# Kernel optimization log

Measured on AMD Instinct MI355X. Metric: run time of the kernel, lower is better.

## Reference

```python
import jax, jax.numpy as jnp
import numpy as np

N = 100000
E = 1600000
F = 64
THETA = (0.6, -0.4, 0.3, -0.2, 0.1)  # k = 5 polynomial coefficients


def setup_inputs() -> dict:
    key = jax.random.key(0)
    kx, ke = jax.random.split(key)
    x = jax.random.normal(kx, (N, F), dtype=jnp.float32)
    edge_index = jax.random.randint(ke, (2, E), 0, N, dtype=jnp.int64)
    return {"x": x, "edge_index": edge_index}


def _l_sym_mul(feat, src, dst, deg_inv_sqrt, n):
    # L_sym * feat = feat - D^{-1/2} A D^{-1/2} feat
    src_norm = feat[src] * deg_inv_sqrt[src]            # [E, F] gather + scale
    agg = jax.ops.segment_sum(src_norm, dst, num_segments=n)  # scatter-add to dst
    return feat - deg_inv_sqrt * agg


def reference(x, edge_index):
    src, dst = edge_index[0], edge_index[1]
    n = x.shape[0]
    # in-degree from dst, clamp to >= 1, D^{-1/2} as [N, 1]
    deg = jax.ops.segment_sum(jnp.ones((src.shape[0],), dtype=x.dtype), dst,
                              num_segments=n)
    deg = jnp.maximum(deg, 1.0)[:, None]
    deg_inv_sqrt = deg ** -0.5

    h_acc = THETA[0] * x
    feat = x
    for k in range(1, len(THETA)):
        feat = _l_sym_mul(feat, src, dst, deg_inv_sqrt, n)
        h_acc = h_acc + THETA[k] * feat
    return h_acc
```

## Files before the change

kernel.cpp:

```cpp
#include <hip/hip_runtime.h>


constexpr int kF = 64;
constexpr int BSHIFT = 8;
constexpr int NB = 1 << BSHIFT;
constexpr int TILE = 2048;
constexpr int KMAX = 512;

static __device__ __forceinline__ float bfl(unsigned u) {
    return __uint_as_float(u << 16);
}
static __device__ __forceinline__ float bfh(unsigned u) {
    return __uint_as_float(u & 0xffff0000u);
}
static __device__ __forceinline__ unsigned f2bf(float f) {
    unsigned u = __float_as_uint(f);
    return (u + 0x7fffu + ((u >> 16) & 1u)) >> 16;
}
static __device__ __forceinline__ unsigned pack2(float a, float b) {
    return f2bf(a) | (f2bf(b) << 16);
}

__global__ void k_binA(const int* __restrict__ src, const int* __restrict__ dst,
                       unsigned* __restrict__ pairs, int* __restrict__ gcursor,
                       const float4* __restrict__ x4, uint4* __restrict__ xb4,
                       int n8, int E, int K, int cap) {
    __shared__ int hist[KMAX];
    __shared__ int gb[KMAX];
    const int tid = threadIdx.x;
    const long long tb = (long long)blockIdx.x * TILE;
    const int tcount = (int)min((long long)TILE, (long long)E - tb);

    {
        int per = (n8 + gridDim.x - 1) / (int)gridDim.x;
        int b0 = blockIdx.x * per;
        int b1 = min(b0 + per, n8);
        for (int i = b0 + tid; i < b1; i += 512) {
            float4 a = x4[2 * i];
            float4 b = x4[2 * i + 1];
            uint4 o;
            o.x = pack2(a.x, a.y);
            o.y = pack2(a.z, a.w);
            o.z = pack2(b.x, b.y);
            o.w = pack2(b.z, b.w);
            xb4[i] = o;
        }
    }

    hist[tid] = 0;
    __syncthreads();
    int dc[4], sc[4];
    #pragma unroll
    for (int k = 0; k < 4; ++k) {
        int i = tid + k * 512;
        if (i < tcount) {
            dc[k] = dst[tb + i];
            sc[k] = src[tb + i];
            atomicAdd(&hist[dc[k] >> BSHIFT], 1);
        } else {
            dc[k] = -1;
        }
    }
    __syncthreads();
    int hv = hist[tid];
    gb[tid] = (tid < K && hv > 0) ? atomicAdd(&gcursor[tid], hv) : 0;
    hist[tid] = 0;
    __syncthreads();
    #pragma unroll
    for (int k = 0; k < 4; ++k) {
        if (dc[k] >= 0) {
            int d = dc[k];
            int b = d >> BSHIFT;
            int pos = atomicAdd(&hist[b], 1);
            pairs[(size_t)b * cap + gb[b] + pos] =
                ((unsigned)(d & (NB - 1)) << 23) | (unsigned)sc[k];
        }
    }
}

__global__ void k_binB1(const unsigned* __restrict__ pairs, const int* __restrict__ gcursor,
                        int* __restrict__ rp, float* __restrict__ dinv,
                        int N, int E, int K, int cap) {
    __shared__ int gsc[KMAX];
    __shared__ int cnt[NB];
    __shared__ int stmp[NB];
    const int b = blockIdx.x;
    const int tid = threadIdx.x;

    int gv = (tid < K) ? gcursor[tid] : 0;
    gsc[tid] = gv;
    __syncthreads();
    for (int o = 1; o < KMAX; o <<= 1) {
        int t = (tid >= o) ? gsc[tid - o] : 0;
        __syncthreads();
        gsc[tid] += t;
        __syncthreads();
    }
    const int ecnt = gcursor[b];
    const int base = gsc[b] - ecnt;
    const unsigned* bp = pairs + (size_t)b * cap;

    if (tid < NB) cnt[tid] = 0;
    __syncthreads();
    for (int i = tid; i < ecnt; i += 512)
        atomicAdd(&cnt[bp[i] >> 23], 1);
    __syncthreads();
    int v = (tid < NB) ? cnt[tid] : 0;
    if (tid < NB) stmp[tid] = v;
    __syncthreads();
    for (int o = 1; o < NB; o <<= 1) {
        int t = (tid >= o && tid < NB) ? stmp[tid - o] : 0;
        __syncthreads();
        if (tid < NB) stmp[tid] += t;
        __syncthreads();
    }
    int node = (b << BSHIFT) + tid;
    if (tid < NB && node < N) {
        rp[node] = base + stmp[tid] - v;
        dinv[node] = rsqrtf(fmaxf((float)v, 1.0f));
    }
    if (b == K - 1 && tid == 0) rp[N] = E;
}

__global__ void k_binB2(const unsigned* __restrict__ pairs, const int* __restrict__ gcursor,
                        const int* __restrict__ rp, const float* __restrict__ dinv,
                        int2* __restrict__ ecsr, int N, int K, int cap) {
    __shared__ int cur[NB];
    const int b = blockIdx.x;
    const int tid = threadIdx.x;
    const int ecnt = gcursor[b];
    const unsigned* bp = pairs + (size_t)b * cap;

    int node = (b << BSHIFT) + tid;
    if (tid < NB) cur[tid] = (node < N) ? rp[node] : 0;
    __syncthreads();
    for (int i = tid; i < ecnt; i += 512) {
        unsigned p = bp[i];
        int s = (int)(p & 0x7FFFFFu);
        int pos = atomicAdd(&cur[p >> 23], 1);
        ecsr[pos] = make_int2(s, __float_as_int(dinv[s]));
    }
}

__global__ void k_gather(const int* __restrict__ rp, const int2* __restrict__ ecsr,
                         const unsigned short* __restrict__ featin,
                         const float* __restrict__ dinv,
                         unsigned short* __restrict__ featout, int n) {
    int wid = (blockIdx.x * blockDim.x + threadIdx.x) >> 6;
    int lane = threadIdx.x & 63;
    int half = lane >> 5;
    int r = (lane >> 3) & 3;
    int c = lane & 7;
    int node = wid * 2 + half;
    if (wid * 2 >= n) return;
    bool valid = node < n;
    int beg = valid ? rp[node] : 0;
    int end = valid ? rp[node + 1] : 0;
    int len = end - beg;
    int olen = __shfl_xor(len, 32, 64);
    int mlen = (len > olen) ? len : olen;

    float acc[8] = {0.f, 0.f, 0.f, 0.f, 0.f, 0.f, 0.f, 0.f};
    for (int i = 0; i < mlen; i += 16) {
        int j1 = beg + i + r;
        int j2 = j1 + 4;
        int j3 = j1 + 8;
        int j4 = j1 + 12;
        bool ok1 = j1 < end, ok2 = j2 < end, ok3 = j3 < end, ok4 = j4 < end;
        int2 e1 = ecsr[ok1 ? j1 : 0];
        int2 e2 = ecsr[ok2 ? j2 : 0];
        int2 e3 = ecsr[ok3 ? j3 : 0];
        int2 e4 = ecsr[ok4 ? j4 : 0];
        float w1 = ok1 ? __int_as_float(e1.y) : 0.0f;
        float w2 = ok2 ? __int_as_float(e2.y) : 0.0f;
        float w3 = ok3 ? __int_as_float(e3.y) : 0.0f;
        float w4 = ok4 ? __int_as_float(e4.y) : 0.0f;
        uint4 ra = *(const uint4*)(featin + ((size_t)e1.x << 6) + (c << 3));
        uint4 rb = *(const uint4*)(featin + ((size_t)e2.x << 6) + (c << 3));
        uint4 rc = *(const uint4*)(featin + ((size_t)e3.x << 6) + (c << 3));
        uint4 rd = *(const uint4*)(featin + ((size_t)e4.x << 6) + (c << 3));
        acc[0] += w1 * bfl(ra.x); acc[1] += w1 * bfh(ra.x);
        acc[2] += w1 * bfl(ra.y); acc[3] += w1 * bfh(ra.y);
        acc[4] += w1 * bfl(ra.z); acc[5] += w1 * bfh(ra.z);
        acc[6] += w1 * bfl(ra.w); acc[7] += w1 * bfh(ra.w);
        acc[0] += w2 * bfl(rb.x); acc[1] += w2 * bfh(rb.x);
        acc[2] += w2 * bfl(rb.y); acc[3] += w2 * bfh(rb.y);
        acc[4] += w2 * bfl(rb.z); acc[5] += w2 * bfh(rb.z);
        acc[6] += w2 * bfl(rb.w); acc[7] += w2 * bfh(rb.w);
        acc[0] += w3 * bfl(rc.x); acc[1] += w3 * bfh(rc.x);
        acc[2] += w3 * bfl(rc.y); acc[3] += w3 * bfh(rc.y);
        acc[4] += w3 * bfl(rc.z); acc[5] += w3 * bfh(rc.z);
        acc[6] += w3 * bfl(rc.w); acc[7] += w3 * bfh(rc.w);
        acc[0] += w4 * bfl(rd.x); acc[1] += w4 * bfh(rd.x);
        acc[2] += w4 * bfl(rd.y); acc[3] += w4 * bfh(rd.y);
        acc[4] += w4 * bfl(rd.z); acc[5] += w4 * bfh(rd.z);
        acc[6] += w4 * bfl(rd.w); acc[7] += w4 * bfh(rd.w);
    }
    #pragma unroll
    for (int m = 8; m <= 16; m <<= 1) {
        #pragma unroll
        for (int i = 0; i < 8; ++i)
            acc[i] += __shfl_xor(acc[i], m, 64);
    }

    if (r == 0 && valid) {
        size_t off = ((size_t)node << 6) + (c << 3);
        uint4 rr = *(const uint4*)(featin + off);
        float di = dinv[node];
        uint4 o;
        o.x = pack2(bfl(rr.x) - di * acc[0], bfh(rr.x) - di * acc[1]);
        o.y = pack2(bfl(rr.y) - di * acc[2], bfh(rr.y) - di * acc[3]);
        o.z = pack2(bfl(rr.z) - di * acc[4], bfh(rr.z) - di * acc[5]);
        o.w = pack2(bfl(rr.w) - di * acc[6], bfh(rr.w) - di * acc[7]);
        *(uint4*)(featout + off) = o;
    }
}

__global__ void k_final(const uint4* __restrict__ xb,
                        const uint4* __restrict__ f1, const uint4* __restrict__ f2,
                        const uint4* __restrict__ f3, const uint4* __restrict__ f4,
                        float4* __restrict__ h4, int n8,
                        float t0, float t1, float t2, float t3, float t4) {
    int i = blockIdx.x * blockDim.x + threadIdx.x;
    if (i >= n8) return;
    uint4 xv = xb[i];
    uint4 a = f1[i], b = f2[i], cc = f3[i], d = f4[i];
    float4 h0, h1;
    h0.x = t0 * bfl(xv.x) + t1 * bfl(a.x) + t2 * bfl(b.x) + t3 * bfl(cc.x) + t4 * bfl(d.x);
    h0.y = t0 * bfh(xv.x) + t1 * bfh(a.x) + t2 * bfh(b.x) + t3 * bfh(cc.x) + t4 * bfh(d.x);
    h0.z = t0 * bfl(xv.y) + t1 * bfl(a.y) + t2 * bfl(b.y) + t3 * bfl(cc.y) + t4 * bfl(d.y);
    h0.w = t0 * bfh(xv.y) + t1 * bfh(a.y) + t2 * bfh(b.y) + t3 * bfh(cc.y) + t4 * bfh(d.y);
    h1.x = t0 * bfl(xv.z) + t1 * bfl(a.z) + t2 * bfl(b.z) + t3 * bfl(cc.z) + t4 * bfl(d.z);
    h1.y = t0 * bfh(xv.z) + t1 * bfh(a.z) + t2 * bfh(b.z) + t3 * bfh(cc.z) + t4 * bfh(d.z);
    h1.z = t0 * bfl(xv.w) + t1 * bfl(a.w) + t2 * bfl(b.w) + t3 * bfl(cc.w) + t4 * bfl(d.w);
    h1.w = t0 * bfh(xv.w) + t1 * bfh(a.w) + t2 * bfh(b.w) + t3 * bfh(cc.w) + t4 * bfh(d.w);
    h4[2 * i] = h0;
    h4[2 * i + 1] = h1;
}

extern "C" void kernel_launch(void* const* d_in, const int* in_sizes, int n_in,
                              void* d_out, int out_size, void* d_ws, size_t ws_size,
                              hipStream_t stream) {
    const float* x  = (const float*)d_in[0];
    const int*   ei = (const int*)d_in[1];
    const int N = in_sizes[0] / kF;
    const int E = in_sizes[1] / 2;
    const int* src = ei;
    const int* dst = ei + E;
    float* h = (float*)d_out;

    const int K = (N + NB - 1) >> BSHIFT;
    const int cap = 2 * ((E + K - 1) / K);

    char* ws = (char*)d_ws;
    size_t off = 0;
    auto carve = [&](size_t bytes) {
        void* p = ws + off;
        off = (off + bytes + 511) & ~(size_t)511;
        return p;
    };
    int*            gcursor = (int*)carve((size_t)K * 4);
    int*            rp      = (int*)carve((size_t)(N + 1) * 4);
    float*          dinv    = (float*)carve((size_t)N * 4);
    int2*           ecsr    = (int2*)carve((size_t)E * 8);
    unsigned short* xb      = (unsigned short*)carve((size_t)N * kF * 2);
    unsigned short* f1      = (unsigned short*)carve((size_t)N * kF * 2);
    unsigned short* f2      = (unsigned short*)carve((size_t)N * kF * 2);
    unsigned short* f3      = (unsigned short*)carve((size_t)N * kF * 2);
    unsigned short* f4      = (unsigned short*)carve((size_t)N * kF * 2);
    unsigned*       pairs   = (unsigned*)carve((size_t)K * cap * 4);

    const float theta[5] = {0.6f, -0.4f, 0.3f, -0.2f, 0.1f};
    const int n8 = N * kF / 8;

    hipMemsetAsync(gcursor, 0, (size_t)K * 4, stream);
    k_binA<<<(E + TILE - 1) / TILE, 512, 0, stream>>>(src, dst, pairs, gcursor,
                                                      (const float4*)x, (uint4*)xb,
                                                      n8, E, K, cap);
    k_binB1<<<K, 512, 0, stream>>>(pairs, gcursor, rp, dinv, N, E, K, cap);
    k_binB2<<<K, 512, 0, stream>>>(pairs, gcursor, rp, dinv, ecsr, N, K, cap);

    const int nwaves = (N + 1) / 2;
    const int gblocks = (nwaves + 3) / 4;
    k_gather<<<gblocks, 256, 0, stream>>>(rp, ecsr, xb, dinv, f1, N);
    k_gather<<<gblocks, 256, 0, stream>>>(rp, ecsr, f1, dinv, f2, N);
    k_gather<<<gblocks, 256, 0, stream>>>(rp, ecsr, f2, dinv, f3, N);
    k_gather<<<gblocks, 256, 0, stream>>>(rp, ecsr, f3, dinv, f4, N);

    k_final<<<(n8 + 255) / 256, 256, 0, stream>>>((const uint4*)xb,
                                                  (const uint4*)f1, (const uint4*)f2,
                                                  (const uint4*)f3, (const uint4*)f4,
                                                  (float4*)h, n8,
                                                  theta[0], theta[1], theta[2],
                                                  theta[3], theta[4]);
}
```

Before: 268.0 us.

## Sort nodes by degree for balanced gather and halve per-iteration unroll

Adds a counting sort of nodes by in-degree (histogram, scan, permutation kernels) and has each gather wave process nodes in descending-degree order. Half-waves paired together then have similar edge counts, which reduces idle lanes from the max-length loop. The inner loop now handles 8 edges per iteration instead of 16, so less work is wasted on masked slots. In exchange it launches three extra small kernels, and output writes and self-feature reads become scattered through the permutation.

```diff
diff --git a/kernel.cpp b/kernel.cpp
--- a/kernel.cpp
+++ b/kernel.cpp
@@ -142,7 +142,64 @@
     }
 }
 
-__global__ void k_gather(const int* __restrict__ rp, const int2* __restrict__ ecsr,
+__global__ void k_dhist(const int* __restrict__ rp, int* __restrict__ dhist, int N) {
+    __shared__ int lh[64];
+    int tid = threadIdx.x;
+    int node = blockIdx.x * 256 + tid;
+    if (tid < 64) lh[tid] = 0;
+    __syncthreads();
+    if (node < N) {
+        int d = rp[node + 1] - rp[node];
+        atomicAdd(&lh[63 - min(d, 63)], 1);
+    }
+    __syncthreads();
+    if (tid < 64 && lh[tid] > 0) atomicAdd(&dhist[tid], lh[tid]);
+}
+
+__global__ void k_dscan(const int* __restrict__ dhist, int* __restrict__ dcur) {
+    __shared__ int t[64];
+    int tid = threadIdx.x;
+    int v = dhist[tid];
+    t[tid] = v;
+    __syncthreads();
+    for (int o = 1; o < 64; o <<= 1) {
+        int u = (tid >= o) ? t[tid - o] : 0;
+        __syncthreads();
+        t[tid] += u;
+        __syncthreads();
+    }
+    dcur[tid] = t[tid] - v;
+}
+
+__global__ void k_dperm(const int* __restrict__ rp, int* __restrict__ dcur,
+                        int* __restrict__ perm, int N) {
+    __shared__ int lh[64];
+    __shared__ int lbase[64];
+    __shared__ int lcur[64];
+    int tid = threadIdx.x;
+    int node = blockIdx.x * 256 + tid;
+    if (tid < 64) lh[tid] = 0;
+    __syncthreads();
+    int bin = -1;
+    if (node < N) {
+        int d = rp[node + 1] - rp[node];
+        bin = 63 - min(d, 63);
+        atomicAdd(&lh[bin], 1);
+    }
+    __syncthreads();
+    if (tid < 64) {
+        lbase[tid] = atomicAdd(&dcur[tid], lh[tid]);
+        lcur[tid] = 0;
+    }
+    __syncthreads();
+    if (bin >= 0) {
+        int pos = lbase[bin] + atomicAdd(&lcur[bin], 1);
+        perm[pos] = node;
+    }
+}
+
+__global__ void k_gather(const int* __restrict__ perm, const int* __restrict__ rp,
+                         const int2* __restrict__ ecsr,
                          const unsigned short* __restrict__ featin,
                          const float* __restrict__ dinv,
                          unsigned short* __restrict__ featout, int n) {
@@ -151,9 +208,10 @@
     int half = lane >> 5;
     int r = (lane >> 3) & 3;
     int c = lane & 7;
-    int node = wid * 2 + half;
+    int idx = wid * 2 + half;
     if (wid * 2 >= n) return;
-    bool valid = node < n;
+    bool valid = idx < n;
+    int node = valid ? perm[idx] : 0;
     int beg = valid ? rp[node] : 0;
     int end = valid ? rp[node + 1] : 0;
     int len = end - beg;
@@ -161,24 +219,17 @@
     int mlen = (len > olen) ? len : olen;
 
     float acc[8] = {0.f, 0.f, 0.f, 0.f, 0.f, 0.f, 0.f, 0.f};
-    for (int i = 0; i < mlen; i += 16) {
+    for (int i = 0; i < mlen; i += 8) {
         int j1 = beg + i + r;
         int j2 = j1 + 4;
-        int j3 = j1 + 8;
-        int j4 = j1 + 12;
-        bool ok1 = j1 < end, ok2 = j2 < end, ok3 = j3 < end, ok4 = j4 < end;
+        bool ok1 = j1 < end;
+        bool ok2 = j2 < end;
         int2 e1 = ecsr[ok1 ? j1 : 0];
         int2 e2 = ecsr[ok2 ? j2 : 0];
-        int2 e3 = ecsr[ok3 ? j3 : 0];
-        int2 e4 = ecsr[ok4 ? j4 : 0];
         float w1 = ok1 ? __int_as_float(e1.y) : 0.0f;
         float w2 = ok2 ? __int_as_float(e2.y) : 0.0f;
-        float w3 = ok3 ? __int_as_float(e3.y) : 0.0f;
-        float w4 = ok4 ? __int_as_float(e4.y) : 0.0f;
         uint4 ra = *(const uint4*)(featin + ((size_t)e1.x << 6) + (c << 3));
         uint4 rb = *(const uint4*)(featin + ((size_t)e2.x << 6) + (c << 3));
-        uint4 rc = *(const uint4*)(featin + ((size_t)e3.x << 6) + (c << 3));
-        uint4 rd = *(const uint4*)(featin + ((size_t)e4.x << 6) + (c << 3));
         acc[0] += w1 * bfl(ra.x); acc[1] += w1 * bfh(ra.x);
         acc[2] += w1 * bfl(ra.y); acc[3] += w1 * bfh(ra.y);
         acc[4] += w1 * bfl(ra.z); acc[5] += w1 * bfh(ra.z);
@@ -187,14 +238,6 @@
         acc[2] += w2 * bfl(rb.y); acc[3] += w2 * bfh(rb.y);
         acc[4] += w2 * bfl(rb.z); acc[5] += w2 * bfh(rb.z);
         acc[6] += w2 * bfl(rb.w); acc[7] += w2 * bfh(rb.w);
-        acc[0] += w3 * bfl(rc.x); acc[1] += w3 * bfh(rc.x);
-        acc[2] += w3 * bfl(rc.y); acc[3] += w3 * bfh(rc.y);
-        acc[4] += w3 * bfl(rc.z); acc[5] += w3 * bfh(rc.z);
-        acc[6] += w3 * bfl(rc.w); acc[7] += w3 * bfh(rc.w);
-        acc[0] += w4 * bfl(rd.x); acc[1] += w4 * bfh(rd.x);
-        acc[2] += w4 * bfl(rd.y); acc[3] += w4 * bfh(rd.y);
-        acc[4] += w4 * bfl(rd.z); acc[5] += w4 * bfh(rd.z);
-        acc[6] += w4 * bfl(rd.w); acc[7] += w4 * bfh(rd.w);
     }
     #pragma unroll
     for (int m = 8; m <= 16; m <<= 1) {
@@ -259,7 +302,10 @@
         off = (off + bytes + 511) & ~(size_t)511;
         return p;
     };
-    int*            gcursor = (int*)carve((size_t)K * 4);
+    int*            gcursor = (int*)carve((size_t)(K + 64) * 4);
+    int*            dhist   = gcursor + K;
+    int*            dcur    = (int*)carve(64 * 4);
+    int*            perm    = (int*)carve((size_t)N * 4);
     int*            rp      = (int*)carve((size_t)(N + 1) * 4);
     float*          dinv    = (float*)carve((size_t)N * 4);
     int2*           ecsr    = (int2*)carve((size_t)E * 8);
@@ -272,20 +318,25 @@
 
     const float theta[5] = {0.6f, -0.4f, 0.3f, -0.2f, 0.1f};
     const int n8 = N * kF / 8;
-
-    hipMemsetAsync(gcursor, 0, (size_t)K * 4, stream);
+    const int nblk = (N + 255) / 256;
+
+    hipMemsetAsync(gcursor, 0, (size_t)(K + 64) * 4, stream);
     k_binA<<<(E + TILE - 1) / TILE, 512, 0, stream>>>(src, dst, pairs, gcursor,
                                                       (const float4*)x, (uint4*)xb,
                                                       n8, E, K, cap);
     k_binB1<<<K, 512, 0, stream>>>(pairs, gcursor, rp, dinv, N, E, K, cap);
     k_binB2<<<K, 512, 0, stream>>>(pairs, gcursor, rp, dinv, ecsr, N, K, cap);
 
+    k_dhist<<<nblk, 256, 0, stream>>>(rp, dhist, N);
+    k_dscan<<<1, 64, 0, stream>>>(dhist, dcur);
+    k_dperm<<<nblk, 256, 0, stream>>>(rp, dcur, perm, N);
+
     const int nwaves = (N + 1) / 2;
     const int gblocks = (nwaves + 3) / 4;
-    k_gather<<<gblocks, 256, 0, stream>>>(rp, ecsr, xb, dinv, f1, N);
-    k_gather<<<gblocks, 256, 0, stream>>>(rp, ecsr, f1, dinv, f2, N);
-    k_gather<<<gblocks, 256, 0, stream>>>(rp, ecsr, f2, dinv, f3, N);
-    k_gather<<<gblocks, 256, 0, stream>>>(rp, ecsr, f3, dinv, f4, N);
+    k_gather<<<gblocks, 256, 0, stream>>>(perm, rp, ecsr, xb, dinv, f1, N);
+    k_gather<<<gblocks, 256, 0, stream>>>(perm, rp, ecsr, f1, dinv, f2, N);
+    k_gather<<<gblocks, 256, 0, stream>>>(perm, rp, ecsr, f2, dinv, f3, N);
+    k_gather<<<gblocks, 256, 0, stream>>>(perm, rp, ecsr, f3, dinv, f4, N);
 
     k_final<<<(n8 + 255) / 256, 256, 0, stream>>>((const uint4*)xb,
                                                   (const uint4*)f1, (const uint4*)f2,
```

New measurement: 301.9 us. +12.7%, slower.

## Rescale features by D^-1/2 so gather uses unweighted index-only CSR

Applied to the files above, without the earlier changes.

The propagation is rewritten in terms of g = D^{-1/2} f, so each gather sums raw neighbour rows and scales by 1/deg, and the final combine multiplies back by sqrt(deg). This lets the CSR hold only 4-byte source indices instead of (index, weight) pairs, which halves edge-list traffic and folds the two binning kernels into one. An extra k_g0 pass is added, and the pairs buffer now aliases g4. The gather unroll drops from 4 to 2 edges per lane, which reduces memory-level parallelism, and the bf16 rounding of the scaled values changes numerics slightly.

```diff
diff --git a/kernel.cpp b/kernel.cpp
--- a/kernel.cpp
+++ b/kernel.cpp
@@ -78,12 +78,14 @@
     }
 }
 
-__global__ void k_binB1(const unsigned* __restrict__ pairs, const int* __restrict__ gcursor,
-                        int* __restrict__ rp, float* __restrict__ dinv,
-                        int N, int E, int K, int cap) {
+__global__ void k_binB(const unsigned* __restrict__ pairs, const int* __restrict__ gcursor,
+                       int* __restrict__ rp, float* __restrict__ dinv,
+                       float* __restrict__ dinv2, float* __restrict__ rdeg,
+                       int* __restrict__ csr, int N, int E, int K, int cap) {
     __shared__ int gsc[KMAX];
     __shared__ int cnt[NB];
     __shared__ int stmp[NB];
+    __shared__ int cur[NB];
     const int b = blockIdx.x;
     const int tid = threadIdx.x;
 
@@ -115,37 +117,44 @@
         __syncthreads();
     }
     int node = (b << BSHIFT) + tid;
-    if (tid < NB && node < N) {
-        rp[node] = base + stmp[tid] - v;
-        dinv[node] = rsqrtf(fmaxf((float)v, 1.0f));
+    if (tid < NB) {
+        int abs0 = base + stmp[tid] - v;
+        cur[tid] = abs0;
+        if (node < N) {
+            rp[node] = abs0;
+            float d = fmaxf((float)v, 1.0f);
+            dinv[node]  = rsqrtf(d);
+            dinv2[node] = 1.0f / d;
+            rdeg[node]  = sqrtf(d);
+        }
     }
     if (b == K - 1 && tid == 0) rp[N] = E;
-}
-
-__global__ void k_binB2(const unsigned* __restrict__ pairs, const int* __restrict__ gcursor,
-                        const int* __restrict__ rp, const float* __restrict__ dinv,
-                        int2* __restrict__ ecsr, int N, int K, int cap) {
-    __shared__ int cur[NB];
-    const int b = blockIdx.x;
-    const int tid = threadIdx.x;
-    const int ecnt = gcursor[b];
-    const unsigned* bp = pairs + (size_t)b * cap;
-
-    int node = (b << BSHIFT) + tid;
-    if (tid < NB) cur[tid] = (node < N) ? rp[node] : 0;
     __syncthreads();
     for (int i = tid; i < ecnt; i += 512) {
         unsigned p = bp[i];
-        int s = (int)(p & 0x7FFFFFu);
         int pos = atomicAdd(&cur[p >> 23], 1);
-        ecsr[pos] = make_int2(s, __float_as_int(dinv[s]));
-    }
-}
-
-__global__ void k_gather(const int* __restrict__ rp, const int2* __restrict__ ecsr,
-                         const unsigned short* __restrict__ featin,
-                         const float* __restrict__ dinv,
-                         unsigned short* __restrict__ featout, int n) {
+        csr[pos] = (int)(p & 0x7FFFFFu);
+    }
+}
+
+__global__ void k_g0(const uint4* __restrict__ xb, const float* __restrict__ dinv,
+                     uint4* __restrict__ g0, int n8) {
+    int i = blockIdx.x * blockDim.x + threadIdx.x;
+    if (i >= n8) return;
+    float di = dinv[i >> 3];
+    uint4 xv = xb[i];
+    uint4 o;
+    o.x = pack2(di * bfl(xv.x), di * bfh(xv.x));
+    o.y = pack2(di * bfl(xv.y), di * bfh(xv.y));
+    o.z = pack2(di * bfl(xv.z), di * bfh(xv.z));
+    o.w = pack2(di * bfl(xv.w), di * bfh(xv.w));
+    g0[i] = o;
+}
+
+__global__ void k_gather(const int* __restrict__ rp, const int* __restrict__ csr,
+                         const unsigned short* __restrict__ gin,
+                         const float* __restrict__ dinv2,
+                         unsigned short* __restrict__ gout, int n) {
     int wid = (blockIdx.x * blockDim.x + threadIdx.x) >> 6;
     int lane = threadIdx.x & 63;
     int half = lane >> 5;
@@ -161,24 +170,17 @@
     int mlen = (len > olen) ? len : olen;
 
     float acc[8] = {0.f, 0.f, 0.f, 0.f, 0.f, 0.f, 0.f, 0.f};
-    for (int i = 0; i < mlen; i += 16) {
+    for (int i = 0; i < mlen; i += 8) {
         int j1 = beg + i + r;
         int j2 = j1 + 4;
-        int j3 = j1 + 8;
-        int j4 = j1 + 12;
-        bool ok1 = j1 < end, ok2 = j2 < end, ok3 = j3 < end, ok4 = j4 < end;
-        int2 e1 = ecsr[ok1 ? j1 : 0];
-        int2 e2 = ecsr[ok2 ? j2 : 0];
-        int2 e3 = ecsr[ok3 ? j3 : 0];
-        int2 e4 = ecsr[ok4 ? j4 : 0];
-        float w1 = ok1 ? __int_as_float(e1.y) : 0.0f;
-        float w2 = ok2 ? __int_as_float(e2.y) : 0.0f;
-        float w3 = ok3 ? __int_as_float(e3.y) : 0.0f;
-        float w4 = ok4 ? __int_as_float(e4.y) : 0.0f;
-        uint4 ra = *(const uint4*)(featin + ((size_t)e1.x << 6) + (c << 3));
-        uint4 rb = *(const uint4*)(featin + ((size_t)e2.x << 6) + (c << 3));
-        uint4 rc = *(const uint4*)(featin + ((size_t)e3.x << 6) + (c << 3));
-        uint4 rd = *(const uint4*)(featin + ((size_t)e4.x << 6) + (c << 3));
+        bool ok1 = j1 < end;
+        bool ok2 = j2 < end;
+        int s1 = csr[ok1 ? j1 : 0];
+        int s2 = csr[ok2 ? j2 : 0];
+        float w1 = ok1 ? 1.0f : 0.0f;
+        float w2 = ok2 ? 1.0f : 0.0f;
+        uint4 ra = *(const uint4*)(gin + ((size_t)s1 << 6) + (c << 3));
+        uint4 rb = *(const uint4*)(gin + ((size_t)s2 << 6) + (c << 3));
         acc[0] += w1 * bfl(ra.x); acc[1] += w1 * bfh(ra.x);
         acc[2] += w1 * bfl(ra.y); acc[3] += w1 * bfh(ra.y);
         acc[4] += w1 * bfl(ra.z); acc[5] += w1 * bfh(ra.z);
@@ -187,14 +189,6 @@
         acc[2] += w2 * bfl(rb.y); acc[3] += w2 * bfh(rb.y);
         acc[4] += w2 * bfl(rb.z); acc[5] += w2 * bfh(rb.z);
         acc[6] += w2 * bfl(rb.w); acc[7] += w2 * bfh(rb.w);
-        acc[0] += w3 * bfl(rc.x); acc[1] += w3 * bfh(rc.x);
-        acc[2] += w3 * bfl(rc.y); acc[3] += w3 * bfh(rc.y);
-        acc[4] += w3 * bfl(rc.z); acc[5] += w3 * bfh(rc.z);
-        acc[6] += w3 * bfl(rc.w); acc[7] += w3 * bfh(rc.w);
-        acc[0] += w4 * bfl(rd.x); acc[1] += w4 * bfh(rd.x);
-        acc[2] += w4 * bfl(rd.y); acc[3] += w4 * bfh(rd.y);
-        acc[4] += w4 * bfl(rd.z); acc[5] += w4 * bfh(rd.z);
-        acc[6] += w4 * bfl(rd.w); acc[7] += w4 * bfh(rd.w);
     }
     #pragma unroll
     for (int m = 8; m <= 16; m <<= 1) {
@@ -205,35 +199,37 @@
 
     if (r == 0 && valid) {
         size_t off = ((size_t)node << 6) + (c << 3);
-        uint4 rr = *(const uint4*)(featin + off);
-        float di = dinv[node];
+        uint4 rr = *(const uint4*)(gin + off);
+        float d2 = dinv2[node];
         uint4 o;
-        o.x = pack2(bfl(rr.x) - di * acc[0], bfh(rr.x) - di * acc[1]);
-        o.y = pack2(bfl(rr.y) - di * acc[2], bfh(rr.y) - di * acc[3]);
-        o.z = pack2(bfl(rr.z) - di * acc[4], bfh(rr.z) - di * acc[5]);
-        o.w = pack2(bfl(rr.w) - di * acc[6], bfh(rr.w) - di * acc[7]);
-        *(uint4*)(featout + off) = o;
-    }
-}
-
-__global__ void k_final(const uint4* __restrict__ xb,
-                        const uint4* __restrict__ f1, const uint4* __restrict__ f2,
-                        const uint4* __restrict__ f3, const uint4* __restrict__ f4,
+        o.x = pack2(bfl(rr.x) - d2 * acc[0], bfh(rr.x) - d2 * acc[1]);
+        o.y = pack2(bfl(rr.y) - d2 * acc[2], bfh(rr.y) - d2 * acc[3]);
+        o.z = pack2(bfl(rr.z) - d2 * acc[4], bfh(rr.z) - d2 * acc[5]);
+        o.w = pack2(bfl(rr.w) - d2 * acc[6], bfh(rr.w) - d2 * acc[7]);
+        *(uint4*)(gout + off) = o;
+    }
+}
+
+__global__ void k_final(const uint4* __restrict__ xb, const float* __restrict__ rdeg,
+                        const uint4* __restrict__ g1, const uint4* __restrict__ g2,
+                        const uint4* __restrict__ g3, const uint4* __restrict__ g4,
                         float4* __restrict__ h4, int n8,
                         float t0, float t1, float t2, float t3, float t4) {
     int i = blockIdx.x * blockDim.x + threadIdx.x;
     if (i >= n8) return;
+    float rd = rdeg[i >> 3];
+    float s1 = rd * t1, s2 = rd * t2, s3 = rd * t3, s4 = rd * t4;
     uint4 xv = xb[i];
-    uint4 a = f1[i], b = f2[i], cc = f3[i], d = f4[i];
+    uint4 a = g1[i], b = g2[i], cc = g3[i], d = g4[i];
     float4 h0, h1;
-    h0.x = t0 * bfl(xv.x) + t1 * bfl(a.x) + t2 * bfl(b.x) + t3 * bfl(cc.x) + t4 * bfl(d.x);
-    h0.y = t0 * bfh(xv.x) + t1 * bfh(a.x) + t2 * bfh(b.x) + t3 * bfh(cc.x) + t4 * bfh(d.x);
-    h0.z = t0 * bfl(xv.y) + t1 * bfl(a.y) + t2 * bfl(b.y) + t3 * bfl(cc.y) + t4 * bfl(d.y);
-    h0.w = t0 * bfh(xv.y) + t1 * bfh(a.y) + t2 * bfh(b.y) + t3 * bfh(cc.y) + t4 * bfh(d.y);
-    h1.x = t0 * bfl(xv.z) + t1 * bfl(a.z) + t2 * bfl(b.z) + t3 * bfl(cc.z) + t4 * bfl(d.z);
-    h1.y = t0 * bfh(xv.z) + t1 * bfh(a.z) + t2 * bfh(b.z) + t3 * bfh(cc.z) + t4 * bfh(d.z);
-    h1.z = t0 * bfl(xv.w) + t1 * bfl(a.w) + t2 * bfl(b.w) + t3 * bfl(cc.w) + t4 * bfl(d.w);
-    h1.w = t0 * bfh(xv.w) + t1 * bfh(a.w) + t2 * bfh(b.w) + t3 * bfh(cc.w) + t4 * bfh(d.w);
+    h0.x = t0 * bfl(xv.x) + s1 * bfl(a.x) + s2 * bfl(b.x) + s3 * bfl(cc.x) + s4 * bfl(d.x);
+    h0.y = t0 * bfh(xv.x) + s1 * bfh(a.x) + s2 * bfh(b.x) + s3 * bfh(cc.x) + s4 * bfh(d.x);
+    h0.z = t0 * bfl(xv.y) + s1 * bfl(a.y) + s2 * bfl(b.y) + s3 * bfl(cc.y) + s4 * bfl(d.y);
+    h0.w = t0 * bfh(xv.y) + s1 * bfh(a.y) + s2 * bfh(b.y) + s3 * bfh(cc.y) + s4 * bfh(d.y);
+    h1.x = t0 * bfl(xv.z) + s1 * bfl(a.z) + s2 * bfl(b.z) + s3 * bfl(cc.z) + s4 * bfl(d.z);
+    h1.y = t0 * bfh(xv.z) + s1 * bfh(a.z) + s2 * bfh(b.z) + s3 * bfh(cc.z) + s4 * bfh(d.z);
+    h1.z = t0 * bfl(xv.w) + s1 * bfl(a.w) + s2 * bfl(b.w) + s3 * bfl(cc.w) + s4 * bfl(d.w);
+    h1.w = t0 * bfh(xv.w) + s1 * bfh(a.w) + s2 * bfh(b.w) + s3 * bfh(cc.w) + s4 * bfh(d.w);
     h4[2 * i] = h0;
     h4[2 * i + 1] = h1;
 }
@@ -262,13 +258,16 @@
     int*            gcursor = (int*)carve((size_t)K * 4);
     int*            rp      = (int*)carve((size_t)(N + 1) * 4);
     float*          dinv    = (float*)carve((size_t)N * 4);
-    int2*           ecsr    = (int2*)carve((size_t)E * 8);
+    float*          dinv2   = (float*)carve((size_t)N * 4);
+    float*          rdeg    = (float*)carve((size_t)N * 4);
+    int*            csr     = (int*)carve((size_t)E * 4);
     unsigned short* xb      = (unsigned short*)carve((size_t)N * kF * 2);
-    unsigned short* f1      = (unsigned short*)carve((size_t)N * kF * 2);
-    unsigned short* f2      = (unsigned short*)carve((size_t)N * kF * 2);
-    unsigned short* f3      = (unsigned short*)carve((size_t)N * kF * 2);
-    unsigned short* f4      = (unsigned short*)carve((size_t)N * kF * 2);
-    unsigned*       pairs   = (unsigned*)carve((size_t)K * cap * 4);
+    unsigned short* g0      = (unsigned short*)carve((size_t)N * kF * 2);
+    unsigned short* g1      = (unsigned short*)carve((size_t)N * kF * 2);
+    unsigned short* g2      = (unsigned short*)carve((size_t)N * kF * 2);
+    unsigned short* g3      = (unsigned short*)carve((size_t)N * kF * 2);
+    unsigned short* g4      = (unsigned short*)carve((size_t)N * kF * 2);
+    unsigned*       pairs   = (unsigned*)g4;
 
     const float theta[5] = {0.6f, -0.4f, 0.3f, -0.2f, 0.1f};
     const int n8 = N * kF / 8;
@@ -277,19 +276,20 @@
     k_binA<<<(E + TILE - 1) / TILE, 512, 0, stream>>>(src, dst, pairs, gcursor,
                                                       (const float4*)x, (uint4*)xb,
                                                       n8, E, K, cap);
-    k_binB1<<<K, 512, 0, stream>>>(pairs, gcursor, rp, dinv, N, E, K, cap);
-    k_binB2<<<K, 512, 0, stream>>>(pairs, gcursor, rp, dinv, ecsr, N, K, cap);
+    k_binB<<<K, 512, 0, stream>>>(pairs, gcursor, rp, dinv, dinv2, rdeg, csr,
+                                  N, E, K, cap);
+    k_g0<<<(n8 + 255) / 256, 256, 0, stream>>>((const uint4*)xb, dinv, (uint4*)g0, n8);
 
     const int nwaves = (N + 1) / 2;
     const int gblocks = (nwaves + 3) / 4;
-    k_gather<<<gblocks, 256, 0, stream>>>(rp, ecsr, xb, dinv, f1, N);
-    k_gather<<<gblocks, 256, 0, stream>>>(rp, ecsr, f1, dinv, f2, N);
-    k_gather<<<gblocks, 256, 0, stream>>>(rp, ecsr, f2, dinv, f3, N);
-    k_gather<<<gblocks, 256, 0, stream>>>(rp, ecsr, f3, dinv, f4, N);
-
-    k_final<<<(n8 + 255) / 256, 256, 0, stream>>>((const uint4*)xb,
-                                                  (const uint4*)f1, (const uint4*)f2,
-                                                  (const uint4*)f3, (const uint4*)f4,
+    k_gather<<<gblocks, 256, 0, stream>>>(rp, csr, g0, dinv2, g1, N);
+    k_gather<<<gblocks, 256, 0, stream>>>(rp, csr, g1, dinv2, g2, N);
+    k_gather<<<gblocks, 256, 0, stream>>>(rp, csr, g2, dinv2, g3, N);
+    k_gather<<<gblocks, 256, 0, stream>>>(rp, csr, g3, dinv2, g4, N);
+
+    k_final<<<(n8 + 255) / 256, 256, 0, stream>>>((const uint4*)xb, rdeg,
+                                                  (const uint4*)g1, (const uint4*)g2,
+                                                  (const uint4*)g3, (const uint4*)g4,
                                                   (float4*)h, n8,
                                                   theta[0], theta[1], theta[2],
                                                   theta[3], theta[4]);
```

After: 267.2 us. No clear change (-0.3%).
